# Kernel tuning notes

Hardware: AMD Instinct MI355X
Metric: run time of the kernel (lower is better)

Reference implementation:

```python
import jax, jax.numpy as jnp
import numpy as np

E = 5        # num_experts
K = 2        # top-k routing
DIM = 768    # token dim
HID = 3072   # dim * mlp_ratio
T = 16384    # num tokens (batch*seq collapsed, per SparseDispatcher contract)
EPS = float(np.finfo(np.float64).eps)  # np.finfo(float).eps used in combine


def setup_inputs() -> dict:
    key = jax.random.key(0)
    ks = jax.random.split(key, 5)
    x = jax.random.normal(ks[0], (T, DIM), jnp.float32)
    # w_gate is nn.Parameter(zeros) in the source; randomize so routing is non-trivial
    w_gate = jax.random.normal(ks[1], (DIM, E), jnp.float32) * 0.02
    # stacked ExpertMLP params (fc1: dim->hid, fc2: hid->dim), small init per init_weights
    W1 = jax.random.normal(ks[2], (E, DIM, HID), jnp.float32) * 0.02
    b1 = jnp.zeros((E, HID), jnp.float32)
    W2 = jax.random.normal(ks[3], (E, HID, DIM), jnp.float32) * 0.02
    b2 = jnp.zeros((E, DIM), jnp.float32)
    return {"x": x, "w_gate": w_gate, "W1": W1, "b1": b1, "W2": W2, "b2": b2}


def reference(x, w_gate, W1, b1, W2, b2):
    # --- noisy top-k gating, eval mode (no noise added at inference) ---
    logits = x @ w_gate                              # [T, E]
    top_vals, top_idx = jax.lax.top_k(logits, K)     # [T, K]
    top_gates = jax.nn.softmax(top_vals, axis=-1)    # softmax over selected logits
    tok = jnp.arange(x.shape[0])[:, None]
    gates = jnp.zeros_like(logits).at[tok, top_idx].set(top_gates)  # sparse [T, E]

    # --- dispatch / expert MLP / combine ---
    # SparseDispatcher.combine: combined[b] = log(sum_e gate[b,e] * exp(expert_e(x[b])))
    # (zeros where no expert contributes are replaced by eps before log)
    acc = jnp.zeros((x.shape[0], DIM), jnp.float32)
    for e in range(E):  # small fixed expert count; dense-equivalent of sparse dispatch
        h = jax.nn.gelu(x @ W1[e] + b1[e], approximate=False)  # torch nn.GELU (erf)
        y = h @ W2[e] + b2[e]                                   # [T, DIM]
        acc = acc + gates[:, e:e + 1] * jnp.exp(y)
    return jnp.log(jnp.where(acc == 0.0, EPS, acc))
```

## Files before the change

### kernel.cpp

```cpp
#include <hip/hip_runtime.h>
#include <math.h>

#define T_TOK 16384
#define DIM   768
#define HID   3072
#define NE    5
#define MT    65
#define HCAP  (MT * 128)
#define CSTR  32
#define EPSF  2.2204460492503131e-16f
#define NXCD  8

typedef short bf16x8  __attribute__((ext_vector_type(8)));
typedef float f32x4   __attribute__((ext_vector_type(4)));
typedef float f32x16  __attribute__((ext_vector_type(16)));

#define MFMA16(A, B, C) __builtin_amdgcn_mfma_f32_16x16x32_bf16((A), (B), (C), 0, 0, 0)
#define MFMA32(A, B, C) __builtin_amdgcn_mfma_f32_32x32x16_bf16((A), (B), (C), 0, 0, 0)

__device__ __forceinline__ unsigned short f2bf(float f) {
    unsigned int u = __float_as_uint(f);
    unsigned int r = (u + 0x7fffu + ((u >> 16) & 1u)) >> 16;
    return (unsigned short)r;
}

__device__ __forceinline__ void gld16(const void* g, void* l) {
    __builtin_amdgcn_global_load_lds(
        (const __attribute__((address_space(1))) void*)g,
        (__attribute__((address_space(3))) void*)l, 16, 0, 0);
}

__global__ void prep_w1p(const float* __restrict__ W1, unsigned short* __restrict__ W1p) {
    int idx = blockIdx.x * 256 + threadIdx.x;
    if (idx >= NE * 24 * 12 * 128 * 8) return;
    int p = idx & 7;
    int n = (idx >> 3) & 127;
    int t = idx >> 10;
    int kb = t % 12; t /= 12;
    int nb = t % 24; int e = t / 24;
    int klog = kb * 64 + (p ^ (n & 7)) * 8;
    const float* src = W1 + ((size_t)e * DIM + klog) * HID + nb * 128 + n;
    bf16x8 v;
    #pragma unroll
    for (int j = 0; j < 8; ++j) v[j] = (short)f2bf(src[(size_t)j * HID]);
    *reinterpret_cast<bf16x8*>(W1p + (size_t)idx * 8) = v;
}

__global__ void prep_w2p(const float* __restrict__ W2, unsigned short* __restrict__ W2p) {
    int idx = blockIdx.x * 256 + threadIdx.x;
    if (idx >= NE * 6 * 48 * 128 * 8) return;
    int p = idx & 7;
    int n = (idx >> 3) & 127;
    int t = idx >> 10;
    int kb = t % 48; t /= 48;
    int nb = t % 6; int e = t / 6;
    int klog = kb * 64 + (p ^ (n & 7)) * 8;
    const float* src = W2 + ((size_t)e * HID + klog) * DIM + nb * 128 + n;
    bf16x8 v;
    #pragma unroll
    for (int j = 0; j < 8; ++j) v[j] = (short)f2bf(src[(size_t)j * DIM]);
    *reinterpret_cast<bf16x8*>(W2p + (size_t)idx * 8) = v;
}

__global__ __launch_bounds__(256) void gate_kernel(
    const float* __restrict__ x, const float* __restrict__ wg,
    unsigned short* __restrict__ xb, int* __restrict__ counts,
    int* __restrict__ btok, float* __restrict__ bgate) {
    __shared__ int   s_e[2][64];
    __shared__ float s_g[2][64];
    __shared__ int   lcnt[NE];
    __shared__ int   gbase[NE];

    const int tid = threadIdx.x;
    if (tid < NE) lcnt[tid] = 0;
    const int grp = tid >> 4, l16 = tid & 15;
    const int t0 = blockIdx.x * 64 + grp * 4;

    double acc[4][NE];
    #pragma unroll
    for (int tt = 0; tt < 4; ++tt)
        #pragma unroll
        for (int e = 0; e < NE; ++e) acc[tt][e] = 0.0;

    for (int i = 0; i < 12; ++i) {
        const int dbase = i * 64 + l16 * 4;
        float4 xv[4];
        #pragma unroll
        for (int tt = 0; tt < 4; ++tt) {
            xv[tt] = *reinterpret_cast<const float4*>(x + (size_t)(t0 + tt) * DIM + dbase);
            ushort4 o;
            o.x = f2bf(xv[tt].x); o.y = f2bf(xv[tt].y);
            o.z = f2bf(xv[tt].z); o.w = f2bf(xv[tt].w);
            *reinterpret_cast<ushort4*>(xb + (size_t)(t0 + tt) * DIM + dbase) = o;
        }
        #pragma unroll
        for (int j = 0; j < 4; ++j) {
            const int d = dbase + j;
            float w0 = wg[d * NE + 0], w1 = wg[d * NE + 1], w2 = wg[d * NE + 2];
            float w3 = wg[d * NE + 3], w4 = wg[d * NE + 4];
            #pragma unroll
            for (int tt = 0; tt < 4; ++tt) {
                double xd = (double)((&xv[tt].x)[j]);
                acc[tt][0] += xd * (double)w0;
                acc[tt][1] += xd * (double)w1;
                acc[tt][2] += xd * (double)w2;
                acc[tt][3] += xd * (double)w3;
                acc[tt][4] += xd * (double)w4;
            }
        }
    }
    #pragma unroll
    for (int off = 8; off; off >>= 1)
        #pragma unroll
        for (int tt = 0; tt < 4; ++tt)
            #pragma unroll
            for (int e = 0; e < NE; ++e)
                acc[tt][e] += __shfl_down(acc[tt][e], off, 16);

    if (l16 == 0) {
        #pragma unroll
        for (int tt = 0; tt < 4; ++tt) {
            double v[NE] = {acc[tt][0], acc[tt][1], acc[tt][2], acc[tt][3], acc[tt][4]};
            int i0 = 0;
            for (int e = 1; e < NE; ++e) if (v[e] > v[i0]) i0 = e;
            int i1 = -1;
            for (int e = 0; e < NE; ++e) {
                if (e == i0) continue;
                if (i1 < 0 || v[e] > v[i1]) i1 = e;
            }
            float e1 = expf((float)(v[i1] - v[i0]));
            float g0 = 1.0f / (1.0f + e1);
            int li = grp * 4 + tt;
            s_e[0][li] = i0;  s_g[0][li] = g0;
            s_e[1][li] = i1;  s_g[1][li] = -(e1 * g0);
        }
    }
    __syncthreads();

    int mye = 0, myoff = 0, mytok = 0;
    float myg = 0.0f;
    if (tid < 128) {
        int li = tid >> 1, which = tid & 1;
        mye = s_e[which][li];
        myg = s_g[which][li];
        mytok = blockIdx.x * 64 + li;
        myoff = atomicAdd(&lcnt[mye], 1);
    }
    __syncthreads();
    if (tid < NE) gbase[tid] = atomicAdd(&counts[tid * CSTR], lcnt[tid]);
    __syncthreads();
    if (tid < 128) {
        int p = gbase[mye] + myoff;
        btok[mye * T_TOK + p] = mytok;
        bgate[mye * T_TOK + p] = myg;
    }
}

__global__ __launch_bounds__(256, 4) void combo_kernel(
    const unsigned short* __restrict__ xb,
    const unsigned short* __restrict__ W1p,
    const unsigned short* __restrict__ W2p,
    const float* __restrict__ b1, const float* __restrict__ b2,
    const int* __restrict__ counts, const int* __restrict__ btok,
    const float* __restrict__ bgate,
    unsigned short* __restrict__ h0, unsigned short* __restrict__ h1,
    float* __restrict__ out, float* __restrict__ p1, int g1e, int g2e) {
    __shared__ __align__(16) unsigned short As[128 * 64];
    __shared__ __align__(16) unsigned short Bs[128 * 64];
    __shared__ int   sst[128];
    __shared__ float ssg[128];

    const int x = blockIdx.x & 7;
    const int i = blockIdx.x >> 3;
    const int NG2 = (g2e >= 0) ? MT : 0;
    const int NG1 = (g1e >= 0) ? MT : 0;
    const int n2x = (x < NG2) ? (((NG2 - 1 - x) >> 3) + 1) : 0;
    const int n1x = (x < NG1) ? (((NG1 - 1 - x) >> 3) + 1) : 0;
    bool isG2; int e, mt, nt;
    if (i < n2x * 6) {
        isG2 = true;  e = g2e; mt = x + 8 * (i / 6);  nt = i % 6;
    } else {
        int ii = i - n2x * 6;
        if (ii >= n1x * 24) return;
        isG2 = false; e = g1e; mt = x + 8 * (ii / 24); nt = ii % 24;
    }
    const int cnt = counts[e * CSTR];
    const int m0 = mt * 128;
    if (m0 >= cnt) return;
    unsigned short* hbuf = (e & 1) ? h1 : h0;

    const int tid = threadIdx.x;
    const int wv = tid >> 6, lane = tid & 63;
    const int wm = wv >> 1, wn = wv & 1;
    const int col = lane & 15, quad = lane >> 4;
    const int l8 = lane & 7, r8 = lane >> 3;

    const unsigned short* aptr[4];
    if (isG2) {
        if (tid < 128) {
            int pos = m0 + tid;
            sst[tid] = (pos < cnt) ? btok[e * T_TOK + pos] : -1;
            ssg[tid] = (pos < cnt) ? bgate[e * T_TOK + pos] : 0.0f;
        }
        #pragma unroll
        for (int q = 0; q < 4; ++q) {
            int r = wv * 32 + q * 8 + r8;
            aptr[q] = hbuf + (size_t)(m0 + r) * HID + (l8 ^ r8) * 8;
        }
    } else {
        #pragma unroll
        for (int q = 0; q < 4; ++q) {
            int r = wv * 32 + q * 8 + r8;
            int pos = m0 + r;
            int tok = btok[e * T_TOK + (pos < cnt ? pos : 0)];
            aptr[q] = xb + (size_t)tok * DIM + (l8 ^ r8) * 8;
        }
    }
    const unsigned short* btile = isG2
        ? W2p + ((size_t)(e * 6 + nt)) * 48 * 8192
        : W1p + ((size_t)(e * 24 + nt)) * 12 * 8192;
    const int ksteps = isG2 ? 48 : 12;

    f32x4 acc[4][4];
    #pragma unroll
    for (int i2 = 0; i2 < 4; ++i2)
        #pragma unroll
        for (int j = 0; j < 4; ++j)
            acc[i2][j] = (f32x4){0.f, 0.f, 0.f, 0.f};

    for (int ks = 0; ks < ksteps; ++ks) {
        const unsigned short* bk = btile + (size_t)ks * 8192 + (size_t)wv * 2048 + lane * 8;
        #pragma unroll
        for (int q = 0; q < 4; ++q)
            gld16(aptr[q] + ks * 64, &As[(wv * 4 + q) * 512]);
        #pragma unroll
        for (int q = 0; q < 4; ++q)
            gld16(bk + q * 512, &Bs[(wv * 4 + q) * 512]);
        __syncthreads();
        #pragma unroll
        for (int kf = 0; kf < 2; ++kf) {
            const int p = ((kf * 4 + quad) ^ l8) * 8;
            bf16x8 a[4], b[4];
            #pragma unroll
            for (int i2 = 0; i2 < 4; ++i2)
                a[i2] = *reinterpret_cast<const bf16x8*>(&As[(wm * 64 + i2 * 16 + col) * 64 + p]);
            #pragma unroll
            for (int i2 = 0; i2 < 4; ++i2)
                b[i2] = *reinterpret_cast<const bf16x8*>(&Bs[(wn * 64 + i2 * 16 + col) * 64 + p]);
            #pragma unroll
            for (int i2 = 0; i2 < 4; ++i2)
                #pragma unroll
                for (int j = 0; j < 4; ++j)
                    acc[i2][j] = MFMA16(a[i2], b[j], acc[i2][j]);
        }
        __syncthreads();
    }

    const int nb0 = nt * 128 + wn * 64;
    if (!isG2) {
        #pragma unroll
        for (int j = 0; j < 4; ++j) {
            float bias = b1[e * HID + nb0 + j * 16 + col];
            #pragma unroll
            for (int i2 = 0; i2 < 4; ++i2) {
                #pragma unroll
                for (int r = 0; r < 4; ++r) {
                    int row = m0 + wm * 64 + i2 * 16 + quad * 4 + r;
                    float v = acc[i2][j][r] + bias;
                    float gl = 0.5f * v * (1.0f + erff(v * 0.70710678118654752f));
                    hbuf[(size_t)row * HID + nb0 + j * 16 + col] = f2bf(gl);
                }
            }
        }
    } else {
        #pragma unroll
        for (int j = 0; j < 4; ++j) {
            float bias = b2[e * DIM + nb0 + j * 16 + col];
            #pragma unroll
            for (int i2 = 0; i2 < 4; ++i2) {
                #pragma unroll
                for (int r = 0; r < 4; ++r) {
                    int lrow = wm * 64 + i2 * 16 + quad * 4 + r;
                    int tok = sst[lrow];
                    if (tok >= 0) {
                        float graw = ssg[lrow];
                        float g = fabsf(graw);
                        float v = acc[i2][j][r] + bias;
                        size_t off = (size_t)tok * DIM + nb0 + j * 16 + col;
                        if (p1) {
                            float val = (g > 0.0f) ? g * expf(v) : 0.0f;
                            float* dst = (__float_as_uint(graw) >> 31) ? p1 : out;
                            dst[off] = val;
                        } else if (g > 0.0f) {
                            atomicAdd(out + off, g * expf(v));
                        }
                    }
                }
            }
        }
    }
}

__global__ void log_kernel(float* __restrict__ out, int n4) {
    int i = blockIdx.x * 256 + threadIdx.x;
    if (i < n4) {
        float4 v = reinterpret_cast<float4*>(out)[i];
        v.x = logf(v.x == 0.0f ? EPSF : v.x);
        v.y = logf(v.y == 0.0f ? EPSF : v.y);
        v.z = logf(v.z == 0.0f ? EPSF : v.z);
        v.w = logf(v.w == 0.0f ? EPSF : v.w);
        reinterpret_cast<float4*>(out)[i] = v;
    }
}

__global__ void log2_kernel(float* __restrict__ out, const float* __restrict__ p1, int n4) {
    int i = blockIdx.x * 256 + threadIdx.x;
    if (i < n4) {
        float4 a = reinterpret_cast<float4*>(out)[i];
        float4 b = reinterpret_cast<const float4*>(p1)[i];
        float sx = a.x + b.x, sy = a.y + b.y, sz = a.z + b.z, sw = a.w + b.w;
        a.x = logf(sx == 0.0f ? EPSF : sx);
        a.y = logf(sy == 0.0f ? EPSF : sy);
        a.z = logf(sz == 0.0f ? EPSF : sz);
        a.w = logf(sw == 0.0f ? EPSF : sw);
        reinterpret_cast<float4*>(out)[i] = a;
    }
}

__global__ void prep_w1_v2(const float* __restrict__ W1, unsigned short* __restrict__ W1s) {
    int g = blockIdx.x * 4 + (threadIdx.x >> 6);
    int lane = threadIdx.x & 63;
    int kf = g % 48;
    int rest = g / 48;
    int nt2 = rest % 96;
    int e = rest / 96;
    int n = nt2 * 32 + (lane & 31);
    int k0 = kf * 16 + (lane >> 5) * 8;
    const float* src = W1 + ((size_t)e * DIM + k0) * HID + n;
    bf16x8 v;
    #pragma unroll
    for (int j = 0; j < 8; ++j) v[j] = (short)f2bf(src[(size_t)j * HID]);
    *reinterpret_cast<bf16x8*>(W1s + ((size_t)g * 64 + lane) * 8) = v;
}

__global__ void prep_w2_v2(const float* __restrict__ W2, unsigned short* __restrict__ W2s) {
    int g = blockIdx.x * 4 + (threadIdx.x >> 6);
    int lane = threadIdx.x & 63;
    int kf = g % 192;
    int rest = g / 192;
    int nt2 = rest % 24;
    int e = rest / 24;
    int n = nt2 * 32 + (lane & 31);
    int k0 = kf * 16 + (lane >> 5) * 8;
    const float* src = W2 + ((size_t)e * HID + k0) * DIM + n;
    bf16x8 v;
    #pragma unroll
    for (int j = 0; j < 8; ++j) v[j] = (short)f2bf(src[(size_t)j * DIM]);
    *reinterpret_cast<bf16x8*>(W2s + ((size_t)g * 64 + lane) * 8) = v;
}

__global__ __launch_bounds__(512, 2) void expert_v2(
    const unsigned short* __restrict__ xb, const unsigned short* __restrict__ W1s,
    const unsigned short* __restrict__ W2s, const float* __restrict__ b1,
    const float* __restrict__ b2, const int* __restrict__ counts,
    const int* __restrict__ btok, const float* __restrict__ bgate,
    float* __restrict__ out) {
    __shared__ __align__(16) unsigned short xs[64][776];
    __shared__ __align__(16) unsigned short hs[2][64][136];
    __shared__ int   st[64];
    __shared__ float sg[64];

    const int e = blockIdx.y;
    const int cnt = counts[e * CSTR];
    const int m0 = blockIdx.x * 64;
    if (m0 >= cnt) return;

    const int tid = threadIdx.x;
    const int wv = tid >> 6, lane = tid & 63;
    const int l31 = lane & 31, lhi = lane >> 5;

    if (tid < 64) {
        int pos = m0 + tid;
        st[tid] = (pos < cnt) ? btok[e * T_TOK + pos] : 0;
        sg[tid] = (pos < cnt) ? fabsf(bgate[e * T_TOK + pos]) : 0.0f;
    }
    __syncthreads();
    {
        int r = tid >> 3, seg = tid & 7;
        const unsigned short* src = xb + (size_t)st[r] * DIM + seg * 96;
        unsigned short* dst = &xs[r][seg * 96];
        #pragma unroll
        for (int i = 0; i < 12; ++i)
            reinterpret_cast<bf16x8*>(dst)[i] = reinterpret_cast<const bf16x8*>(src)[i];
    }
    __syncthreads();

    const int mt2 = wv & 1, nt2l = wv >> 1;
    f32x16 acc[2][3];
    #pragma unroll
    for (int a_ = 0; a_ < 2; ++a_)
        #pragma unroll
        for (int b_ = 0; b_ < 3; ++b_)
            #pragma unroll
            for (int q = 0; q < 16; ++q) acc[a_][b_][q] = 0.0f;

    const unsigned short* arow = &xs[mt2 * 32 + l31][lhi * 8];
    for (int jc = 0; jc < 24; ++jc) {
        f32x16 c0, c1;
        #pragma unroll
        for (int q = 0; q < 16; ++q) { c0[q] = 0.0f; c1[q] = 0.0f; }
        const unsigned short* bpa =
            W1s + ((size_t)((e * 96 + jc * 4 + nt2l) * 48)) * 512 + lane * 8;
        #pragma unroll
        for (int kf = 0; kf < 48; kf += 2) {
            bf16x8 a0 = *reinterpret_cast<const bf16x8*>(arow + kf * 16);
            bf16x8 b0 = *reinterpret_cast<const bf16x8*>(bpa + (size_t)kf * 512);
            c0 = MFMA32(a0, b0, c0);
            bf16x8 a1 = *reinterpret_cast<const bf16x8*>(arow + kf * 16 + 16);
            bf16x8 b1 = *reinterpret_cast<const bf16x8*>(bpa + (size_t)kf * 512 + 512);
            c1 = MFMA32(a1, b1, c1);
        }
        #pragma unroll
        for (int q = 0; q < 16; ++q) c0[q] += c1[q];
        {
            int colc = nt2l * 32 + l31;
            float bias = b1[e * HID + jc * 128 + colc];
            #pragma unroll
            for (int reg = 0; reg < 16; ++reg) {
                int row = (reg & 3) + 8 * (reg >> 2) + 4 * lhi;
                float v = c0[reg] + bias;
                float gl = 0.5f * v * (1.0f + erff(v * 0.70710678118654752f));
                hs[jc & 1][mt2 * 32 + row][colc] = f2bf(gl);
            }
        }
        __syncthreads();
        const unsigned short* bpb =
            W2s + ((size_t)((e * 24 + wv * 3) * 192 + jc * 8)) * 512 + lane * 8;
        #pragma unroll
        for (int kf = 0; kf < 8; ++kf) {
            bf16x8 af0 = *reinterpret_cast<const bf16x8*>(&hs[jc & 1][l31][kf * 16 + lhi * 8]);
            bf16x8 af1 = *reinterpret_cast<const bf16x8*>(&hs[jc & 1][32 + l31][kf * 16 + lhi * 8]);
            #pragma unroll
            for (int i = 0; i < 3; ++i) {
                bf16x8 bv = *reinterpret_cast<const bf16x8*>(bpb + ((size_t)i * 192 + kf) * 512);
                acc[0][i] = MFMA32(af0, bv, acc[0][i]);
                acc[1][i] = MFMA32(af1, bv, acc[1][i]);
            }
        }
    }
    #pragma unroll
    for (int mt = 0; mt < 2; ++mt) {
        #pragma unroll
        for (int i = 0; i < 3; ++i) {
            int cg = (wv * 3 + i) * 32 + l31;
            float bias2 = b2[e * DIM + cg];
            #pragma unroll
            for (int reg = 0; reg < 16; ++reg) {
                int row = mt * 32 + (reg & 3) + 8 * (reg >> 2) + 4 * lhi;
                float g = sg[row];
                if (g > 0.0f) {
                    float v = acc[mt][i][reg] + bias2;
                    atomicAdd(out + (size_t)st[row] * DIM + cg, g * expf(v));
                }
            }
        }
    }
}


extern "C" void kernel_launch(void* const* d_in, const int* in_sizes, int n_in,
                              void* d_out, int out_size, void* d_ws, size_t ws_size,
                              hipStream_t stream) {
    const float* x  = (const float*)d_in[0];
    const float* wg = (const float*)d_in[1];
    const float* W1 = (const float*)d_in[2];
    const float* b1 = (const float*)d_in[3];
    const float* W2 = (const float*)d_in[4];
    const float* b2 = (const float*)d_in[5];
    float* out = (float*)d_out;

    char* ws = (char*)d_ws;
    int*            counts = (int*)ws;
    int*            btok   = (int*)(ws + 1024);
    float*          bgate  = (float*)(ws + 1024 + 327680);
    unsigned short* xb     = (unsigned short*)(ws + 1024 + 2 * 327680);
    unsigned short* W1b    = xb + (size_t)T_TOK * DIM;
    unsigned short* W2b    = W1b + (size_t)NE * DIM * HID;
    unsigned short* h0     = W2b + (size_t)NE * HID * DIM;
    unsigned short* h1     = h0 + (size_t)HCAP * HID;
    float*          p1     = (float*)(h1 + (size_t)HCAP * HID);

    const size_t need_fast = 1024 + 2 * 327680
        + (size_t)T_TOK * DIM * 2 + 2 * (size_t)NE * DIM * HID * 2
        + 2 * (size_t)HCAP * HID * 2;
    const size_t need_store = need_fast + (size_t)T_TOK * DIM * 4;
    const bool fast  = ws_size >= need_fast;
    const bool store = ws_size >= need_store;

    hipMemsetAsync(counts, 0, 1024, stream);
    if (!(fast && store))
        hipMemsetAsync(out, 0, (size_t)out_size * sizeof(float), stream);

    gate_kernel<<<T_TOK / 64, 256, 0, stream>>>(x, wg, xb, counts, btok, bgate);

    if (fast) {
        prep_w1p<<<(NE * 24 * 12 * 128 * 8 + 255) / 256, 256, 0, stream>>>(W1, W1b);
        prep_w2p<<<(NE * 6 * 48 * 128 * 8 + 255) / 256, 256, 0, stream>>>(W2, W2b);
        float* p1arg = store ? p1 : nullptr;
        const int gmax = (MT + 7) / 8;
        for (int s = 0; s < 6; ++s) {
            int g1e = (s <= 4) ? s : -1;
            int g2e = s - 1;
            int per_x0 = (g2e >= 0 ? gmax * 6 : 0) + (g1e >= 0 ? gmax * 24 : 0);
            combo_kernel<<<NXCD * per_x0, 256, 0, stream>>>(
                xb, W1b, W2b, b1, b2, counts, btok, bgate, h0, h1, out, p1arg, g1e, g2e);
        }
        if (store)
            log2_kernel<<<(out_size / 4 + 255) / 256, 256, 0, stream>>>(out, p1, out_size / 4);
        else
            log_kernel<<<(out_size / 4 + 255) / 256, 256, 0, stream>>>(out, out_size / 4);
    } else {
        prep_w1_v2<<<NE * 96 * 48 / 4, 256, 0, stream>>>(W1, W1b);
        prep_w2_v2<<<NE * 24 * 192 / 4, 256, 0, stream>>>(W2, W2b);
        expert_v2<<<dim3(T_TOK / 64, NE), 512, 0, stream>>>(
            xb, W1b, W2b, b1, b2, counts, btok, bgate, out);
        log_kernel<<<(out_size / 4 + 255) / 256, 256, 0, stream>>>(out, out_size / 4);
    }
}
```

Measured before the change: 720.7 us.

## Generalize combo launch schedule to pack two jobs per launch with three h buffers

The combo kernel now takes two generic job descriptors (expert plus GEMM1/GEMM2 flag) and a modulus for the hidden-activation buffer ring, instead of a fixed GEMM2(e-1)+GEMM1(e) pairing. When the workspace allows three h buffers plus p1, the host issues five launches that pair two GEMM1s first and then overlap the remaining stages, ending with two GEMM2s together. This removes one launch and its tail bubble in exchange for more workspace memory. The old six-launch schedule is kept as a fallback.

Measured after the change: 727.5 us. No clear change (+1.0%).

```diff
diff --git a/kernel.cpp b/kernel.cpp
--- a/kernel.cpp
+++ b/kernel.cpp
@@ -163,31 +163,34 @@
     const float* __restrict__ b1, const float* __restrict__ b2,
     const int* __restrict__ counts, const int* __restrict__ btok,
     const float* __restrict__ bgate,
-    unsigned short* __restrict__ h0, unsigned short* __restrict__ h1,
-    float* __restrict__ out, float* __restrict__ p1, int g1e, int g2e) {
+    unsigned short* __restrict__ h0,
+    float* __restrict__ out, float* __restrict__ p1,
+    int jA, int jB, int hmod) {
     __shared__ __align__(16) unsigned short As[128 * 64];
     __shared__ __align__(16) unsigned short Bs[128 * 64];
     __shared__ int   sst[128];
     __shared__ float ssg[128];
 
     const int x = blockIdx.x & 7;
-    const int i = blockIdx.x >> 3;
-    const int NG2 = (g2e >= 0) ? MT : 0;
-    const int NG1 = (g1e >= 0) ? MT : 0;
-    const int n2x = (x < NG2) ? (((NG2 - 1 - x) >> 3) + 1) : 0;
-    const int n1x = (x < NG1) ? (((NG1 - 1 - x) >> 3) + 1) : 0;
-    bool isG2; int e, mt, nt;
-    if (i < n2x * 6) {
-        isG2 = true;  e = g2e; mt = x + 8 * (i / 6);  nt = i % 6;
-    } else {
-        int ii = i - n2x * 6;
-        if (ii >= n1x * 24) return;
-        isG2 = false; e = g1e; mt = x + 8 * (ii / 24); nt = ii % 24;
-    }
+    int rem = blockIdx.x >> 3;
+    const int ngx = ((MT - 1 - x) >> 3) + 1;
+    int e = -1; bool isG2 = false; int mt = 0, nt = 0;
+    #pragma unroll
+    for (int s = 0; s < 2; ++s) {
+        int j = (s == 0) ? jA : jB;
+        if (j >= 0 && e < 0) {
+            bool t2 = (j & 8) != 0;
+            int ntl = t2 ? 6 : 24;
+            int sz = ngx * ntl;
+            if (rem < sz) { e = j & 7; isG2 = t2; mt = x + 8 * (rem / ntl); nt = rem % ntl; }
+            else rem -= sz;
+        }
+    }
+    if (e < 0) return;
     const int cnt = counts[e * CSTR];
     const int m0 = mt * 128;
     if (m0 >= cnt) return;
-    unsigned short* hbuf = (e & 1) ? h1 : h0;
+    unsigned short* hbuf = h0 + (size_t)(e % hmod) * HCAP * HID;
 
     const int tid = threadIdx.x;
     const int wv = tid >> 6, lane = tid & 63;
@@ -487,15 +490,17 @@
     unsigned short* W1b    = xb + (size_t)T_TOK * DIM;
     unsigned short* W2b    = W1b + (size_t)NE * DIM * HID;
     unsigned short* h0     = W2b + (size_t)NE * HID * DIM;
-    unsigned short* h1     = h0 + (size_t)HCAP * HID;
-    float*          p1     = (float*)(h1 + (size_t)HCAP * HID);
-
-    const size_t need_fast = 1024 + 2 * 327680
-        + (size_t)T_TOK * DIM * 2 + 2 * (size_t)NE * DIM * HID * 2
-        + 2 * (size_t)HCAP * HID * 2;
-    const size_t need_store = need_fast + (size_t)T_TOK * DIM * 4;
-    const bool fast  = ws_size >= need_fast;
-    const bool store = ws_size >= need_store;
+    const size_t    hsz    = (size_t)HCAP * HID;
+
+    const size_t base_need = 1024 + 2 * 327680
+        + (size_t)T_TOK * DIM * 2 + 2 * (size_t)NE * DIM * HID * 2;
+    const size_t p1sz      = (size_t)T_TOK * DIM * 4;
+    const size_t need_fast  = base_need + 2 * hsz * 2;
+    const size_t need_store = need_fast + p1sz;
+    const size_t need_5     = base_need + 3 * hsz * 2 + p1sz;
+    const bool fast   = ws_size >= need_fast;
+    const bool store  = ws_size >= need_store;
+    const bool five   = ws_size >= need_5;
 
     hipMemsetAsync(counts, 0, 1024, stream);
     if (!(fast && store))
@@ -506,19 +511,38 @@
     if (fast) {
         prep_w1p<<<(NE * 24 * 12 * 128 * 8 + 255) / 256, 256, 0, stream>>>(W1, W1b);
         prep_w2p<<<(NE * 6 * 48 * 128 * 8 + 255) / 256, 256, 0, stream>>>(W2, W2b);
-        float* p1arg = store ? p1 : nullptr;
         const int gmax = (MT + 7) / 8;
-        for (int s = 0; s < 6; ++s) {
-            int g1e = (s <= 4) ? s : -1;
-            int g2e = s - 1;
-            int per_x0 = (g2e >= 0 ? gmax * 6 : 0) + (g1e >= 0 ? gmax * 24 : 0);
-            combo_kernel<<<NXCD * per_x0, 256, 0, stream>>>(
-                xb, W1b, W2b, b1, b2, counts, btok, bgate, h0, h1, out, p1arg, g1e, g2e);
-        }
-        if (store)
+        if (five) {
+            float* p1 = (float*)(h0 + 3 * hsz);
+            const int sched[5][2] = { {0, 1}, {8 | 0, 2}, {8 | 1, 3},
+                                      {8 | 2, 4}, {8 | 3, 8 | 4} };
+            for (int s = 0; s < 5; ++s) {
+                int jA = sched[s][0], jB = sched[s][1];
+                int per_x0 = ((jA & 8) ? gmax * 6 : gmax * 24)
+                           + ((jB & 8) ? gmax * 6 : gmax * 24);
+                combo_kernel<<<NXCD * per_x0, 256, 0, stream>>>(
+                    xb, W1b, W2b, b1, b2, counts, btok, bgate, h0,
+                    out, p1, jA, jB, 3);
+            }
             log2_kernel<<<(out_size / 4 + 255) / 256, 256, 0, stream>>>(out, p1, out_size / 4);
-        else
-            log_kernel<<<(out_size / 4 + 255) / 256, 256, 0, stream>>>(out, out_size / 4);
+        } else {
+            float* p1arg = store ? (float*)(h0 + 2 * hsz) : nullptr;
+            for (int s = 0; s < 6; ++s) {
+                int g1e = (s <= 4) ? s : -1;
+                int g2e = s - 1;
+                int jA = (g2e >= 0) ? (8 | g2e) : -1;
+                int jB = (g1e >= 0) ? g1e : -1;
+                int per_x0 = (g2e >= 0 ? gmax * 6 : 0) + (g1e >= 0 ? gmax * 24 : 0);
+                combo_kernel<<<NXCD * per_x0, 256, 0, stream>>>(
+                    xb, W1b, W2b, b1, b2, counts, btok, bgate, h0,
+                    out, p1arg, jA, jB, 2);
+            }
+            if (store)
+                log2_kernel<<<(out_size / 4 + 255) / 256, 256, 0, stream>>>(
+                    out, (float*)(h0 + 2 * hsz), out_size / 4);
+            else
+                log_kernel<<<(out_size / 4 + 255) / 256, 256, 0, stream>>>(out, out_size / 4);
+        }
     } else {
         prep_w1_v2<<<NE * 96 * 48 / 4, 256, 0, stream>>>(W1, W1b);
         prep_w2_v2<<<NE * 24 * 192 / 4, 256, 0, stream>>>(W2, W2b);
```
